# Kernel tuning notes

Measured on AMD Instinct MI355X. Metric: run time of the kernel, lower is better.

## Reference

```python
import jax, jax.numpy as jnp
import numpy as np

B, N, IN_F, OUT_F = 8, 2048, 256, 256
ALPHA = 0.2  # LeakyReLU negative slope
NEG_INF = -1e9


def setup_inputs() -> dict:
    key = jax.random.key(0)
    ks = jax.random.split(key, 8)
    h = jax.random.normal(ks[0], (B, N, IN_F), dtype=jnp.float32)
    adj = jax.random.randint(ks[1], (B, N, N), 0, 2, dtype=jnp.int32)
    # xavier-ish scaled params
    W_w = jax.random.normal(ks[2], (OUT_F, IN_F), dtype=jnp.float32) * (1.414 / np.sqrt(IN_F + OUT_F))
    W_b = jnp.zeros((OUT_F,), dtype=jnp.float32)
    ai_w = jax.random.normal(ks[3], (1, OUT_F), dtype=jnp.float32) * (1.414 / np.sqrt(OUT_F + 1))
    ai_b = jnp.zeros((1,), dtype=jnp.float32)
    aj_w = jax.random.normal(ks[4], (1, OUT_F), dtype=jnp.float32) * (1.414 / np.sqrt(OUT_F + 1))
    aj_b = jnp.zeros((1,), dtype=jnp.float32)
    return {"h": h, "adj": adj, "W_w": W_w, "W_b": W_b,
            "ai_w": ai_w, "ai_b": ai_b, "aj_w": aj_w, "aj_b": aj_b}


def reference(h, adj, W_w, W_b, ai_w, ai_b, aj_w, aj_b):
    # Wh: [B, N, F]
    Wh = jnp.einsum('bni,oi->bno', h, W_w) + W_b
    # additive attention scores (pos_embed_dim == 1 so the .view is a transpose)
    Wh1 = jnp.einsum('bnf,of->bno', Wh, ai_w) + ai_b        # [B, N, 1]
    Wh2 = jnp.einsum('bnf,of->bno', Wh, aj_w) + aj_b        # [B, N, 1]
    e = Wh1 + jnp.swapaxes(Wh2, 1, 2)                       # [B, N, N]
    e = jnp.where(e >= 0, e, ALPHA * e)                     # LeakyReLU
    attention = jnp.where(adj > 0, e, NEG_INF)
    attention = jax.nn.softmax(attention, axis=2)
    # dropout: inference mode (training=False) -> identity
    h_hat = jnp.einsum('bnm,bmf->bnf', attention, Wh)
    return jax.nn.elu(h_hat)  # concat=True
```

## Files before the change

kernel.cpp:

```cpp
#include <hip/hip_runtime.h>

typedef __bf16 bf16;
typedef _Float16 f16;
typedef __bf16 bf16x8 __attribute__((ext_vector_type(8)));
typedef _Float16 f16x8 __attribute__((ext_vector_type(8)));
typedef float  f32x4  __attribute__((ext_vector_type(4)));

#define B_  8
#define N_  2048
#define F_  256
#define NTOK (B_ * N_)
static constexpr float LOG2E = 1.44269504088896f;

__device__ __forceinline__ int detect_bf16(const void* h) {
    const unsigned* hw = (const unsigned*)h;
    unsigned w = hw[threadIdx.x & 63];
    unsigned ex = (w >> 7) & 0xFFu;
    unsigned long long b = __ballot(ex > 100u && ex < 150u);
    return __popcll(b) >= 40;
}

__device__ __forceinline__ float ldf(const void* p, int i, int isb) {
    return isb ? (float)((const bf16*)p)[i] : ((const float*)p)[i];
}

__device__ __forceinline__ bf16x8 cvt8(const float* p) {
    float4 a = *(const float4*)p;
    float4 b = *(const float4*)(p + 4);
    bf16x8 r;
    r[0]=(bf16)a.x; r[1]=(bf16)a.y; r[2]=(bf16)a.z; r[3]=(bf16)a.w;
    r[4]=(bf16)b.x; r[5]=(bf16)b.y; r[6]=(bf16)b.z; r[7]=(bf16)b.w;
    return r;
}

__global__ __launch_bounds__(256)
void k_wht(const void* __restrict__ hv, const void* __restrict__ Wv,
           const void* __restrict__ Wbv, const void* __restrict__ ai_wv,
           const void* __restrict__ ai_bv, const void* __restrict__ aj_wv,
           const void* __restrict__ aj_bv, bf16* __restrict__ WhT,
           unsigned* __restrict__ adjw) {
    int isb = detect_bf16(hv);
    int ttile = blockIdx.x;
    int fg = threadIdx.x >> 6;
    int lane = threadIdx.x & 63;
    int T0 = ttile * 16;
    int m = lane & 15, quad = lane >> 4;

    f32x4 acc[4];
#pragma unroll
    for (int ft = 0; ft < 4; ++ft) acc[ft] = (f32x4){0.f, 0.f, 0.f, 0.f};

    if (isb) {
        const bf16* hp = (const bf16*)hv + (size_t)(T0 + m) * F_ + quad * 8;
        const bf16* wp = (const bf16*)Wv + (size_t)(fg * 64 + m) * F_ + quad * 8;
#pragma unroll
        for (int kk = 0; kk < F_; kk += 32) {
            bf16x8 hf = *(const bf16x8*)(hp + kk);
#pragma unroll
            for (int ft = 0; ft < 4; ++ft) {
                bf16x8 wf = *(const bf16x8*)(wp + (size_t)ft * 16 * F_ + kk);
                acc[ft] = __builtin_amdgcn_mfma_f32_16x16x32_bf16(wf, hf, acc[ft], 0, 0, 0);
            }
        }
    } else {
        const float* hp = (const float*)hv + (size_t)(T0 + m) * F_ + quad * 8;
        const float* wp = (const float*)Wv + (size_t)(fg * 64 + m) * F_ + quad * 8;
#pragma unroll
        for (int kk = 0; kk < F_; kk += 32) {
            bf16x8 hf = cvt8(hp + kk);
#pragma unroll
            for (int ft = 0; ft < 4; ++ft) {
                bf16x8 wf = cvt8(wp + (size_t)ft * 16 * F_ + kk);
                acc[ft] = __builtin_amdgcn_mfma_f32_16x16x32_bf16(wf, hf, acc[ft], 0, 0, 0);
            }
        }
    }
    int token = T0 + m;
    int b = token >> 11, n = token & (N_ - 1);
    float s_p = 0.f, t_p = 0.f;
#pragma unroll
    for (int ft = 0; ft < 4; ++ft)
#pragma unroll
        for (int r = 0; r < 4; ++r) {
            int f = fg * 64 + ft * 16 + quad * 4 + r;
            float v = acc[ft][r] + ldf(Wbv, f, isb);
            bf16 vb = (bf16)v;
            WhT[((size_t)b * F_ + f) * N_ + n] = vb;
            float vr = (float)vb;
            s_p += vr * ldf(ai_wv, f, isb);
            t_p += vr * ldf(aj_wv, f, isb);
        }
    s_p += __shfl_down(s_p, 32, 64); s_p += __shfl_down(s_p, 16, 64);
    t_p += __shfl_down(t_p, 32, 64); t_p += __shfl_down(t_p, 16, 64);
    __shared__ float sred[4][16], tred[4][16];
    if (lane < 16) { sred[fg][lane] = s_p; tred[fg][lane] = t_p; }
    __syncthreads();
    if (threadIdx.x < 16) {
        int tid = threadIdx.x;
        int tok = T0 + tid;
        float ss = (sred[0][tid] + sred[1][tid] + sred[2][tid] + sred[3][tid]
                    + ldf(ai_bv, 0, isb)) * LOG2E;
        float tt = (tred[0][tid] + tred[1][tid] + tred[2][tid] + tred[3][tid]
                    + ldf(aj_bv, 0, isb)) * LOG2E;
        f16 th = (f16)tt, sh = (f16)ss;
        unsigned short tu, su;
        __builtin_memcpy(&tu, &th, 2);
        __builtin_memcpy(&su, &sh, 2);
        unsigned w0 = adjw[tok];
        adjw[tok] = (w0 & 0xFFFFu) | ((unsigned)tu << 16);
        unsigned w1 = adjw[NTOK + tok];
        adjw[NTOK + tok] = (w1 & 0xFFFFu) | ((unsigned)su << 16);
    }
}

__device__ __forceinline__ unsigned char pbits(uint4 a, uint4 b) {
    return (unsigned char)((a.x & 1u) | ((a.y & 1u) << 1) | ((a.z & 1u) << 2) |
                           ((a.w & 1u) << 3) | ((b.x & 1u) << 4) |
                           ((b.y & 1u) << 5) | ((b.z & 1u) << 6) |
                           ((b.w & 1u) << 7));
}

__device__ __forceinline__ void stageB(const bf16* whb, char* dst, int jc,
                                       int w, int lane) {
    int sl = lane & 7, rsub = lane >> 3;
    int slog = sl ^ rsub;
#pragma unroll
    for (int rr = 0; rr < 4; ++rr) {
        int fr = w * 32 + rr * 8 + rsub;
        const bf16* g = whb + (size_t)fr * N_ + jc + slog * 8;
        __builtin_amdgcn_global_load_lds(
            (const __attribute__((address_space(1))) unsigned*)g,
            (__attribute__((address_space(3))) unsigned*)(dst + (w * 32 + rr * 8) * 128),
            16, 0, 0);
    }
}

__global__ __launch_bounds__(512, 1)
void k_attn(const unsigned* __restrict__ adjw, const bf16* __restrict__ WhT,
            const void* __restrict__ hv, void* __restrict__ outv) {
    int isb = detect_bf16(hv);
    int bid = blockIdx.x;
    int b = bid >> 5, itile = bid & 31, i0 = itile * 64;
    int tid = threadIdx.x;
    int w = tid >> 6, lane = tid & 63, m = lane & 15, q = lane >> 4;
    int mt = w >> 1, jh = w & 1;

    __shared__ __align__(16) char smem[71680];
    char* Bbuf0 = smem;
    char* Bbuf1 = smem + 32768;
    unsigned char* pack0 = (unsigned char*)(smem + 65536);
    unsigned char* pack1 = (unsigned char*)(smem + 66048);
    f16* tLDS   = (f16*)(smem + 66560);
    float* lLDS = (float*)(smem + 70656);
    float* red  = (float*)smem;

    const bf16* whb = WhT + (size_t)b * F_ * N_;

#pragma unroll
    for (int k = 0; k < 4; ++k) {
        int idx = k * 512 + tid;
        unsigned wv = adjw[b * N_ + idx];
        unsigned short us = (unsigned short)(wv >> 16);
        f16 tv; __builtin_memcpy(&tv, &us, 2);
        tLDS[idx] = tv;
    }
    int row = i0 + mt * 16 + m;
    unsigned swd = adjw[NTOK + b * N_ + row];
    unsigned short su = (unsigned short)(swd >> 16);
    f16 sh; __builtin_memcpy(&sh, &su, 2);
    float s2i = (float)sh;

    int prow = tid >> 3, ps = tid & 7;
    {
        const unsigned* ap = adjw + ((size_t)(b * N_ + i0 + prow)) * N_ + ps * 8;
        uint4 x0 = *(const uint4*)ap, x1 = *(const uint4*)(ap + 4);
        pack0[prow * 8 + ps] = pbits(x0, x1);
    }
    stageB(whb, Bbuf0, 0, w, lane);
    __syncthreads();

    f32x4 acc[16];
#pragma unroll
    for (int ft = 0; ft < 16; ++ft) acc[ft] = (f32x4){0.f, 0.f, 0.f, 0.f};
    float lpart = 0.f;

    for (int c = 0; c < 32; ++c) {
        char* Bcur = (c & 1) ? Bbuf1 : Bbuf0;
        unsigned char* pcur = (c & 1) ? pack1 : pack0;
        uint4 aw0, aw1;
        bool pre = (c < 31);
        if (pre) {
            stageB(whb, (c & 1) ? Bbuf0 : Bbuf1, (c + 1) * 64, w, lane);
            const unsigned* ap = adjw + ((size_t)(b * N_ + i0 + prow)) * N_ +
                                 (c + 1) * 64 + ps * 8;
            aw0 = *(const uint4*)ap; aw1 = *(const uint4*)(ap + 4);
        }
        unsigned long long pb64 =
            *(const unsigned long long*)(pcur + (mt * 16 + m) * 8);
        unsigned bits8 = (unsigned)(pb64 >> ((jh * 4 + q) * 8)) & 0xFFu;
        f16x8 tv = *(const f16x8*)(tLDS + c * 64 + jh * 32 + q * 8);

        bf16x8 af;
#pragma unroll
        for (int qq = 0; qq < 8; ++qq) {
            float x = s2i + (float)tv[qq];
            x = fmaxf(x, 0.2f * x);
            float pv = ((bits8 >> qq) & 1u) ? __builtin_amdgcn_exp2f(x) : 0.f;
            bf16 pbv = (bf16)pv;
            af[qq] = pbv;
            lpart += (float)pbv;
        }
        int psw = ((jh * 4 + q) ^ (m & 7)) * 16;
#pragma unroll
        for (int ft = 0; ft < 16; ++ft) {
            int fr = ft * 16 + m;
            bf16x8 bfr = *(const bf16x8*)(Bcur + fr * 128 + psw);
            acc[ft] = __builtin_amdgcn_mfma_f32_16x16x32_bf16(af, bfr, acc[ft], 0, 0, 0);
        }
        if (pre)
            ((c & 1) ? pack0 : pack1)[prow * 8 + ps] = pbits(aw0, aw1);
        __syncthreads();
    }

    lpart += __shfl_down(lpart, 32, 64);
    lpart += __shfl_down(lpart, 16, 64);
    if (lane < 16) lLDS[w * 16 + lane] = lpart;
    if (jh == 1) {
#pragma unroll
        for (int ft = 0; ft < 16; ++ft)
#pragma unroll
            for (int r = 0; r < 4; ++r)
                red[(mt * 16 + q * 4 + r) * 258 + ft * 16 + m] = acc[ft][r];
    }
    __syncthreads();
    if (jh == 0) {
#pragma unroll
        for (int r = 0; r < 4; ++r) {
            int rr = q * 4 + r;
            float lf = lLDS[(mt * 2) * 16 + rr] + lLDS[(mt * 2 + 1) * 16 + rr];
            float rl = (lf > 0.f) ? (1.f / lf) : 0.f;
            size_t ob = ((size_t)b * N_ + i0 + mt * 16 + rr) * F_;
#pragma unroll
            for (int ft = 0; ft < 16; ++ft) {
                int f = ft * 16 + m;
                float v = acc[ft][r] + red[(mt * 16 + rr) * 258 + f];
                v *= rl;
                v = (v > 0.f) ? v : (__builtin_amdgcn_exp2f(v * LOG2E) - 1.f);
                if (isb) ((bf16*)outv)[ob + f] = (bf16)v;
                else     ((float*)outv)[ob + f] = v;
            }
        }
    }
}

extern "C" void kernel_launch(void* const* d_in, const int* in_sizes, int n_in,
                              void* d_out, int out_size, void* d_ws, size_t ws_size,
                              hipStream_t stream) {
    (void)in_sizes; (void)n_in; (void)out_size; (void)ws_size;
    const void* h    = d_in[0];
    unsigned*   adjw = (unsigned*)d_in[1];
    const void* W_w  = d_in[2];
    const void* W_b  = d_in[3];
    const void* ai_w = d_in[4];
    const void* ai_b = d_in[5];
    const void* aj_w = d_in[6];
    const void* aj_b = d_in[7];

    bf16* WhT = (bf16*)d_ws;

    k_wht <<<dim3(1024), dim3(256), 0, stream>>>(h, W_w, W_b, ai_w, ai_b,
                                                 aj_w, aj_b, WhT, adjw);
    k_attn<<<dim3(256),  dim3(512), 0, stream>>>(adjw, WhT, h, d_out);
}
```

Before: 277.8 us.

## Pre-tile swizzled WhT layout, halve attention row tile, sum row weights via MFMA

The projection kernel now writes Wh in a pre-tiled, pre-swizzled layout of contiguous 64-column chunks. The attention kernel can then stage each B tile with fully contiguous global-to-LDS loads. The attention kernel moves to 512 blocks of 256 threads covering 32 rows each, which gives more blocks for the GPU's CUs. The per-lane softmax denominator accumulation and shuffle reduction are replaced by an extra MFMA against a ones vector. The cost is that the WhT tile is re-streamed for half as many rows, doubling B-tile global traffic, and the k_wht output stores become scattered.

```diff
diff --git a/kernel.cpp b/kernel.cpp
--- a/kernel.cpp
+++ b/kernel.cpp
@@ -33,11 +33,17 @@
     return r;
 }
 
+__device__ __forceinline__ size_t wht2_idx(int b, int f, int n) {
+    int jc = n >> 6;
+    int slot = ((n >> 3) & 7) ^ (f & 7);
+    return (((size_t)(b * 32 + jc) * F_ + f) << 6) + (slot << 3) + (n & 7);
+}
+
 __global__ __launch_bounds__(256)
 void k_wht(const void* __restrict__ hv, const void* __restrict__ Wv,
            const void* __restrict__ Wbv, const void* __restrict__ ai_wv,
            const void* __restrict__ ai_bv, const void* __restrict__ aj_wv,
-           const void* __restrict__ aj_bv, bf16* __restrict__ WhT,
+           const void* __restrict__ aj_bv, bf16* __restrict__ WhT2,
            unsigned* __restrict__ adjw) {
     int isb = detect_bf16(hv);
     int ttile = blockIdx.x;
@@ -85,7 +91,7 @@
             int f = fg * 64 + ft * 16 + quad * 4 + r;
             float v = acc[ft][r] + ldf(Wbv, f, isb);
             bf16 vb = (bf16)v;
-            WhT[((size_t)b * F_ + f) * N_ + n] = vb;
+            WhT2[wht2_idx(b, f, n)] = vb;
             float vr = (float)vb;
             s_p += vr * ldf(ai_wv, f, isb);
             t_p += vr * ldf(aj_wv, f, isb);
@@ -120,45 +126,42 @@
                            ((b.w & 1u) << 7));
 }
 
-__device__ __forceinline__ void stageB(const bf16* whb, char* dst, int jc,
+__device__ __forceinline__ void stageB(const bf16* tile, char* dst,
                                        int w, int lane) {
-    int sl = lane & 7, rsub = lane >> 3;
-    int slog = sl ^ rsub;
-#pragma unroll
-    for (int rr = 0; rr < 4; ++rr) {
-        int fr = w * 32 + rr * 8 + rsub;
-        const bf16* g = whb + (size_t)fr * N_ + jc + slog * 8;
+#pragma unroll
+    for (int r = 0; r < 8; ++r) {
+        int off = (w * 8 + r) * 1024;
+        const bf16* g = tile + off / 2 + lane * 8;
         __builtin_amdgcn_global_load_lds(
             (const __attribute__((address_space(1))) unsigned*)g,
-            (__attribute__((address_space(3))) unsigned*)(dst + (w * 32 + rr * 8) * 128),
+            (__attribute__((address_space(3))) unsigned*)(dst + off),
             16, 0, 0);
     }
 }
 
-__global__ __launch_bounds__(512, 1)
-void k_attn(const unsigned* __restrict__ adjw, const bf16* __restrict__ WhT,
+__global__ __launch_bounds__(256)
+void k_attn(const unsigned* __restrict__ adjw, const bf16* __restrict__ WhT2,
             const void* __restrict__ hv, void* __restrict__ outv) {
     int isb = detect_bf16(hv);
     int bid = blockIdx.x;
-    int b = bid >> 5, itile = bid & 31, i0 = itile * 64;
+    int b = bid >> 6, itile = bid & 63, i0 = itile * 32;
     int tid = threadIdx.x;
     int w = tid >> 6, lane = tid & 63, m = lane & 15, q = lane >> 4;
     int mt = w >> 1, jh = w & 1;
 
-    __shared__ __align__(16) char smem[71680];
+    __shared__ __align__(16) char smem[70656];
     char* Bbuf0 = smem;
     char* Bbuf1 = smem + 32768;
-    unsigned char* pack0 = (unsigned char*)(smem + 65536);
-    unsigned char* pack1 = (unsigned char*)(smem + 66048);
-    f16* tLDS   = (f16*)(smem + 66560);
-    float* lLDS = (float*)(smem + 70656);
+    f16* tLDS   = (f16*)(smem + 65536);
+    unsigned char* pack0 = (unsigned char*)(smem + 69632);
+    unsigned char* pack1 = (unsigned char*)(smem + 69888);
     float* red  = (float*)smem;
 
-    const bf16* whb = WhT + (size_t)b * F_ * N_;
-
-#pragma unroll
-    for (int k = 0; k < 4; ++k) {
-        int idx = k * 512 + tid;
+    const bf16* batch_tiles = WhT2 + ((size_t)b * 32) * F_ * 64;
+
+#pragma unroll
+    for (int k = 0; k < 8; ++k) {
+        int idx = k * 256 + tid;
         unsigned wv = adjw[b * N_ + idx];
         unsigned short us = (unsigned short)(wv >> 16);
         f16 tv; __builtin_memcpy(&tv, &us, 2);
@@ -171,18 +174,22 @@
     float s2i = (float)sh;
 
     int prow = tid >> 3, ps = tid & 7;
+    const unsigned* arow = adjw + ((size_t)(b * N_ + i0 + prow)) * N_ + ps * 8;
     {
-        const unsigned* ap = adjw + ((size_t)(b * N_ + i0 + prow)) * N_ + ps * 8;
-        uint4 x0 = *(const uint4*)ap, x1 = *(const uint4*)(ap + 4);
+        uint4 x0 = *(const uint4*)arow, x1 = *(const uint4*)(arow + 4);
         pack0[prow * 8 + ps] = pbits(x0, x1);
     }
-    stageB(whb, Bbuf0, 0, w, lane);
+    stageB(batch_tiles, Bbuf0, w, lane);
     __syncthreads();
 
+    bf16x8 ones;
+#pragma unroll
+    for (int k = 0; k < 8; ++k) ones[k] = (bf16)1.0f;
+
     f32x4 acc[16];
 #pragma unroll
     for (int ft = 0; ft < 16; ++ft) acc[ft] = (f32x4){0.f, 0.f, 0.f, 0.f};
-    float lpart = 0.f;
+    f32x4 acc_l = {0.f, 0.f, 0.f, 0.f};
 
     for (int c = 0; c < 32; ++c) {
         char* Bcur = (c & 1) ? Bbuf1 : Bbuf0;
@@ -190,10 +197,10 @@
         uint4 aw0, aw1;
         bool pre = (c < 31);
         if (pre) {
-            stageB(whb, (c & 1) ? Bbuf0 : Bbuf1, (c + 1) * 64, w, lane);
-            const unsigned* ap = adjw + ((size_t)(b * N_ + i0 + prow)) * N_ +
-                                 (c + 1) * 64 + ps * 8;
-            aw0 = *(const uint4*)ap; aw1 = *(const uint4*)(ap + 4);
+            stageB(batch_tiles + (size_t)(c + 1) * F_ * 64,
+                   (c & 1) ? Bbuf0 : Bbuf1, w, lane);
+            aw0 = *(const uint4*)(arow + (size_t)(c + 1) * 64);
+            aw1 = *(const uint4*)(arow + (size_t)(c + 1) * 64 + 4);
         }
         unsigned long long pb64 =
             *(const unsigned long long*)(pcur + (mt * 16 + m) * 8);
@@ -206,44 +213,44 @@
             float x = s2i + (float)tv[qq];
             x = fmaxf(x, 0.2f * x);
             float pv = ((bits8 >> qq) & 1u) ? __builtin_amdgcn_exp2f(x) : 0.f;
-            bf16 pbv = (bf16)pv;
-            af[qq] = pbv;
-            lpart += (float)pbv;
-        }
-        int psw = ((jh * 4 + q) ^ (m & 7)) * 16;
+            af[qq] = (bf16)pv;
+        }
+        int sbase = (jh * 4 + q);
 #pragma unroll
         for (int ft = 0; ft < 16; ++ft) {
             int fr = ft * 16 + m;
-            bf16x8 bfr = *(const bf16x8*)(Bcur + fr * 128 + psw);
+            int psl = sbase ^ (m & 7);
+            bf16x8 bfr = *(const bf16x8*)(Bcur + fr * 128 + psl * 16);
             acc[ft] = __builtin_amdgcn_mfma_f32_16x16x32_bf16(af, bfr, acc[ft], 0, 0, 0);
         }
+        acc_l = __builtin_amdgcn_mfma_f32_16x16x32_bf16(af, ones, acc_l, 0, 0, 0);
         if (pre)
             ((c & 1) ? pack0 : pack1)[prow * 8 + ps] = pbits(aw0, aw1);
         __syncthreads();
     }
 
-    lpart += __shfl_down(lpart, 32, 64);
-    lpart += __shfl_down(lpart, 16, 64);
-    if (lane < 16) lLDS[w * 16 + lane] = lpart;
     if (jh == 1) {
 #pragma unroll
-        for (int ft = 0; ft < 16; ++ft)
-#pragma unroll
-            for (int r = 0; r < 4; ++r)
-                red[(mt * 16 + q * 4 + r) * 258 + ft * 16 + m] = acc[ft][r];
+        for (int r = 0; r < 4; ++r) {
+            int rr = mt * 16 + q * 4 + r;
+#pragma unroll
+            for (int ft = 0; ft < 16; ++ft)
+                red[rr * 257 + ft * 16 + m] = acc[ft][r];
+            if (m == 0) red[rr * 257 + 256] = acc_l[r];
+        }
     }
     __syncthreads();
     if (jh == 0) {
 #pragma unroll
         for (int r = 0; r < 4; ++r) {
-            int rr = q * 4 + r;
-            float lf = lLDS[(mt * 2) * 16 + rr] + lLDS[(mt * 2 + 1) * 16 + rr];
+            int rr = mt * 16 + q * 4 + r;
+            float lf = acc_l[r] + red[rr * 257 + 256];
             float rl = (lf > 0.f) ? (1.f / lf) : 0.f;
-            size_t ob = ((size_t)b * N_ + i0 + mt * 16 + rr) * F_;
+            size_t ob = ((size_t)b * N_ + i0 + rr) * F_;
 #pragma unroll
             for (int ft = 0; ft < 16; ++ft) {
                 int f = ft * 16 + m;
-                float v = acc[ft][r] + red[(mt * 16 + rr) * 258 + f];
+                float v = acc[ft][r] + red[rr * 257 + f];
                 v *= rl;
                 v = (v > 0.f) ? v : (__builtin_amdgcn_exp2f(v * LOG2E) - 1.f);
                 if (isb) ((bf16*)outv)[ob + f] = (bf16)v;
@@ -266,9 +273,9 @@
     const void* aj_w = d_in[6];
     const void* aj_b = d_in[7];
 
-    bf16* WhT = (bf16*)d_ws;
+    bf16* WhT2 = (bf16*)d_ws;
 
     k_wht <<<dim3(1024), dim3(256), 0, stream>>>(h, W_w, W_b, ai_w, ai_b,
-                                                 aj_w, aj_b, WhT, adjw);
-    k_attn<<<dim3(256),  dim3(512), 0, stream>>>(adjw, WhT, h, d_out);
-}
+                                                 aj_w, aj_b, WhT2, adjw);
+    k_attn<<<dim3(512),  dim3(256), 0, stream>>>(adjw, WhT2, h, d_out);
+}
```

After: 272.2 us. 1.02x faster.
